# Optimization experiments

Measured on AMD Instinct MI355X. Metric: run time of the kernel, lower is better.

## Reference

```python
import jax, jax.numpy as jnp
import numpy as np

N_NODES = 100000
N_EDGES = 1600000
IN_CH, HID_CH, OUT_CH = 128, 64, 64


def setup_inputs() -> dict:
    key = jax.random.key(0)
    ks = jax.random.split(key, 6)
    x = jax.random.normal(ks[0], (N_NODES, IN_CH), dtype=jnp.float32)
    edge_index = jax.random.randint(ks[1], (2, N_EDGES), 0, N_NODES, dtype=jnp.int64)
    W1 = jax.random.normal(ks[2], (IN_CH, HID_CH), dtype=jnp.float32) / np.float32(np.sqrt(IN_CH))
    b1 = jax.random.normal(ks[3], (HID_CH,), dtype=jnp.float32) * 0.01
    W2 = jax.random.normal(ks[4], (HID_CH, OUT_CH), dtype=jnp.float32) / np.float32(np.sqrt(HID_CH))
    b2 = jax.random.normal(ks[5], (OUT_CH,), dtype=jnp.float32) * 0.01
    return {"x": x, "edge_index": edge_index, "W1": W1, "b1": b1, "W2": W2, "b2": b2}


def gcn_conv(x, W, b, src, dst, n_nodes):
    """PyG GCNConv: h = x@W; add self-loops; sym-normalized scatter-add; + bias."""
    h = x @ W  # (N, F_out)
    # degree on graph WITH self-loops (unit edge weights): deg[i] = in-degree + 1
    deg = jax.ops.segment_sum(jnp.ones((src.shape[0],), h.dtype), dst, num_segments=n_nodes) + 1.0
    dinv = jax.lax.rsqrt(deg)  # deg >= 1, no div-by-zero
    norm = dinv[src] * dinv[dst]  # (E,)
    msg = h[src] * norm[:, None]  # (E, F_out) gather + scale
    agg = jax.ops.segment_sum(msg, dst, num_segments=n_nodes)  # scatter-add
    agg = agg + h * (dinv * dinv)[:, None]  # self-loop contribution deg^-1 * h_i
    return agg + b


def reference(x, edge_index, W1, b1, W2, b2):
    src, dst = edge_index[0], edge_index[1]  # source_to_target flow
    n = x.shape[0]
    h = jax.nn.relu(gcn_conv(x, W1, b1, src, dst, n))
    out = gcn_conv(h, W2, b2, src, dst, n)
    return out
```

## Files before the change

### kernel.cpp

```cpp
#include <hip/hip_runtime.h>
#include <hip/hip_fp16.h>


#define CHUNK 2048
#define BCAP  8192
#define NB_PAD 512
#define BSHIFT 8
#define BMASK 255

typedef _Float16 f16x8 __attribute__((ext_vector_type(8)));
typedef float f32x4 __attribute__((ext_vector_type(4)));

__device__ __forceinline__ unsigned int pack2(float a, float b) {
  __half2 h = __floats2half2_rn(a, b);
  return *reinterpret_cast<unsigned int*>(&h);
}
__device__ __forceinline__ __half2 h2add(__half2 a, __half2 b) {
  return __hadd2(a, b);
}
__device__ __forceinline__ __half2 bcast_h2(unsigned int u) {
  return *reinterpret_cast<__half2*>(&u);
}

__global__ __launch_bounds__(256) void initcur_kernel(int* __restrict__ bcursor,
                                                      int nb) {
  int i = blockIdx.x * 256 + threadIdx.x;
  if (i < nb) bcursor[i] = i * BCAP;
}

__global__ __launch_bounds__(512) void chunksort_kernel(
    const int* __restrict__ src, const int* __restrict__ dst,
    int* __restrict__ bcursor, int* __restrict__ ebuck, int nE, int nb) {
  __shared__ int hist[NB_PAD];
  __shared__ int loff[NB_PAD];
  __shared__ int gbase[NB_PAD];
  __shared__ int lcur[NB_PAD];
  __shared__ int part[NB_PAD];
  __shared__ int srec[CHUNK];
  __shared__ int saddr[CHUNK];
  const int t = threadIdx.x;
  const int e0 = blockIdx.x * CHUNK;
  const int n = min(CHUNK, nE - e0);
  hist[t] = 0;
  __syncthreads();
  for (int i = t; i < n; i += 512) atomicAdd(&hist[dst[e0 + i] >> BSHIFT], 1);
  __syncthreads();
  part[t] = hist[t];
  __syncthreads();
  for (int off = 1; off < NB_PAD; off <<= 1) {
    int v = (t >= off) ? part[t - off] : 0;
    __syncthreads();
    part[t] += v;
    __syncthreads();
  }
  int excl = (t == 0) ? 0 : part[t - 1];
  loff[t] = excl;
  if (t < nb) {
    int c = hist[t];
    gbase[t] = c ? atomicAdd(&bcursor[t], c) : 0;
    lcur[t] = excl;
  }
  __syncthreads();
  for (int i = t; i < n; i += 512) {
    int d = dst[e0 + i];
    int b = d >> BSHIFT;
    int p = atomicAdd(&lcur[b], 1);
    srec[p] = src[e0 + i] | ((d & BMASK) << 17);
    saddr[p] = gbase[b] + (p - loff[b]);
  }
  __syncthreads();
  for (int i = t; i < n; i += 512) ebuck[saddr[i]] = srec[i];
}

__global__ __launch_bounds__(1024) void bscan_kernel(const int* __restrict__ bcursor,
                                                     int* __restrict__ bbase, int nb) {
  __shared__ int part[1024];
  const int t = threadIdx.x;
  int c = (t < nb) ? (bcursor[t] - t * BCAP) : 0;
  part[t] = c;
  __syncthreads();
  for (int off = 1; off < 1024; off <<= 1) {
    int v = (t >= off) ? part[t - off] : 0;
    __syncthreads();
    part[t] += v;
    __syncthreads();
  }
  if (t < nb) bbase[t] = part[t] - c;
}

__global__ __launch_bounds__(1024) void bucketsort_kernel(
    const int* __restrict__ ebuck, const int* __restrict__ bcursor,
    const int* __restrict__ bbase, int* __restrict__ esrc,
    int* __restrict__ rowptr, float* __restrict__ dinv, int N, int E, int nb) {
  __shared__ int hist[256];
  __shared__ int sc[256];
  __shared__ int rowcur[256];
  const int t = threadIdx.x;
  const int bk = blockIdx.x;
  const int base = bk * BCAP;
  const int cnt = bcursor[bk] - base;
  const int gb = bbase[bk];
  if (t < 256) hist[t] = 0;
  __syncthreads();
  for (int i = t; i < cnt; i += 1024)
    atomicAdd(&hist[(ebuck[base + i] >> 17) & BMASK], 1);
  __syncthreads();
  if (t < 256) sc[t] = hist[t];
  __syncthreads();
  for (int off = 1; off < 256; off <<= 1) {
    int v = 0;
    if (t < 256 && t >= off) v = sc[t - off];
    __syncthreads();
    if (t < 256) sc[t] += v;
    __syncthreads();
  }
  if (t < 256) {
    int excl = (t == 0) ? 0 : sc[t - 1];
    rowcur[t] = excl;
    int node = bk * 256 + t;
    if (node < N) {
      rowptr[node] = gb + excl;
      dinv[node] = rsqrtf((float)hist[t] + 1.0f);
    }
  }
  if (bk == nb - 1 && t == 0) rowptr[N] = E;
  __syncthreads();
  for (int i = t; i < cnt; i += 1024) {
    int rec = ebuck[base + i];
    int p = atomicAdd(&rowcur[(rec >> 17) & BMASK], 1);
    esrc[gb + p] = rec & 0x1FFFF;
  }
}

template <int K, bool IN_HALF>
__global__ __launch_bounds__(256) void gemm_mfma(const void* __restrict__ Xin,
                                                 const float* __restrict__ W,
                                                 const float* __restrict__ dinv,
                                                 __half* __restrict__ H, int N) {
  __shared__ __align__(16) unsigned char sA[128 * K * 2];
  __shared__ __align__(16) unsigned char sB[64 * K * 2];
  const int t = threadIdx.x;
  const int brow = blockIdx.x * 128;
  constexpr int CH = K / 8;
  for (int idx = t; idx < 128 * CH; idx += 256) {
    int r = idx / CH, c = idx - r * CH;
    int row = brow + r;
    if (row >= N) row = N - 1;
    unsigned int off = (unsigned int)((r * K + c * 8) * 2) ^ ((r & 7) << 4);
    uint4 pk;
    if constexpr (IN_HALF) {
      pk = *reinterpret_cast<const uint4*>((const __half*)Xin + (size_t)row * K + c * 8);
    } else {
      const float4* xp =
          reinterpret_cast<const float4*>((const float*)Xin + (size_t)row * K + c * 8);
      float4 f0 = xp[0], f1 = xp[1];
      pk.x = pack2(f0.x, f0.y);
      pk.y = pack2(f0.z, f0.w);
      pk.z = pack2(f1.x, f1.y);
      pk.w = pack2(f1.z, f1.w);
    }
    *reinterpret_cast<uint4*>(sA + off) = pk;
  }
  for (int idx = t; idx < K * 64; idx += 256) {
    int k = idx >> 6, n = idx & 63;
    __half h = __float2half_rn(W[idx]);
    unsigned int off = (unsigned int)((n * K + k) * 2) ^ ((n & 7) << 4);
    *reinterpret_cast<unsigned short*>(sB + off) =
        *reinterpret_cast<unsigned short*>(&h);
  }
  __syncthreads();

  const int wv = t >> 6, l = t & 63;
  const int lr = l & 15;
  const int lk = (l >> 4) * 8;
  f32x4 acc[2][4] = {};
#pragma unroll
  for (int ks = 0; ks < K / 32; ++ks) {
    f16x8 af[2], bf[4];
#pragma unroll
    for (int m = 0; m < 2; ++m) {
      int r = wv * 32 + m * 16 + lr;
      unsigned int off = (unsigned int)((r * K + ks * 32 + lk) * 2) ^ ((r & 7) << 4);
      af[m] = *reinterpret_cast<const f16x8*>(sA + off);
    }
#pragma unroll
    for (int n = 0; n < 4; ++n) {
      int cc = n * 16 + lr;
      unsigned int off = (unsigned int)((cc * K + ks * 32 + lk) * 2) ^ ((cc & 7) << 4);
      bf[n] = *reinterpret_cast<const f16x8*>(sB + off);
    }
#pragma unroll
    for (int m = 0; m < 2; ++m)
#pragma unroll
      for (int n = 0; n < 4; ++n)
        acc[m][n] = __builtin_amdgcn_mfma_f32_16x16x32_f16(af[m], bf[n], acc[m][n],
                                                           0, 0, 0);
  }
#pragma unroll
  for (int m = 0; m < 2; ++m) {
#pragma unroll
    for (int j = 0; j < 4; ++j) {
      int row = brow + wv * 32 + m * 16 + (l >> 4) * 4 + j;
      if (row < N) {
        float di = dinv[row];
#pragma unroll
        for (int n = 0; n < 4; ++n) {
          float v = acc[m][n][j] * di;
          H[(size_t)row * 64 + n * 16 + lr] = __float2half_rn(v);
        }
      }
    }
  }
}

template <bool RELU, bool OUT_HALF>
__global__ __launch_bounds__(256) void agg_kernel(const __half* __restrict__ hs,
                                                  const int* __restrict__ rowptr,
                                                  const int* __restrict__ esrc,
                                                  const float* __restrict__ dinv,
                                                  const float* __restrict__ b,
                                                  void* __restrict__ outv, int N) {
  const int wv = threadIdx.x >> 6;
  const int lane = threadIdx.x & 63;
  const int nid = lane >> 4;
  const int g = (lane >> 3) & 1;
  const int cl = lane & 7;
  const int node = blockIdx.x * 16 + wv * 4 + nid;
  const unsigned int choff = (unsigned int)cl << 4;
  const unsigned char* __restrict__ hb = (const unsigned char*)hs;
  int beg = 0, end = 0;
  if (node < N) {
    beg = rowptr[node];
    end = rowptr[node + 1];
  }
  __half2 accA[4] = {{0.f, 0.f}, {0.f, 0.f}, {0.f, 0.f}, {0.f, 0.f}};
  __half2 accB[4] = {{0.f, 0.f}, {0.f, 0.f}, {0.f, 0.f}, {0.f, 0.f}};
  int k = beg + g;
  while (k < end) {
    int s0 = esrc[min(k,     end - 1)];
    int s1 = esrc[min(k + 2, end - 1)];
    int s2 = esrc[min(k + 4, end - 1)];
    int s3 = esrc[min(k + 6, end - 1)];
    uint4 v0 = *reinterpret_cast<const uint4*>(hb + (((unsigned int)s0 << 7) + choff));
    uint4 v1 = *reinterpret_cast<const uint4*>(hb + (((unsigned int)s1 << 7) + choff));
    uint4 v2 = *reinterpret_cast<const uint4*>(hb + (((unsigned int)s2 << 7) + choff));
    uint4 v3 = *reinterpret_cast<const uint4*>(hb + (((unsigned int)s3 << 7) + choff));
    {
      accA[0] = h2add(accA[0], bcast_h2(v0.x));
      accA[1] = h2add(accA[1], bcast_h2(v0.y));
      accA[2] = h2add(accA[2], bcast_h2(v0.z));
      accA[3] = h2add(accA[3], bcast_h2(v0.w));
    }
    if (k + 2 < end) {
      accB[0] = h2add(accB[0], bcast_h2(v1.x));
      accB[1] = h2add(accB[1], bcast_h2(v1.y));
      accB[2] = h2add(accB[2], bcast_h2(v1.z));
      accB[3] = h2add(accB[3], bcast_h2(v1.w));
    }
    if (k + 4 < end) {
      accA[0] = h2add(accA[0], bcast_h2(v2.x));
      accA[1] = h2add(accA[1], bcast_h2(v2.y));
      accA[2] = h2add(accA[2], bcast_h2(v2.z));
      accA[3] = h2add(accA[3], bcast_h2(v2.w));
    }
    if (k + 6 < end) {
      accB[0] = h2add(accB[0], bcast_h2(v3.x));
      accB[1] = h2add(accB[1], bcast_h2(v3.y));
      accB[2] = h2add(accB[2], bcast_h2(v3.z));
      accB[3] = h2add(accB[3], bcast_h2(v3.w));
    }
    k += 8;
  }
#pragma unroll
  for (int r = 0; r < 4; ++r) accA[r] = h2add(accA[r], accB[r]);
#pragma unroll
  for (int r = 0; r < 4; ++r) {
    int u = __shfl_xor(*reinterpret_cast<int*>(&accA[r]), 8);
    accA[r] = h2add(accA[r], *reinterpret_cast<__half2*>(&u));
  }
  if (g == 0 && node < N) {
    uint4 sv = *reinterpret_cast<const uint4*>(hb + (((unsigned int)node << 7) + choff));
    float di = dinv[node];
    const float4* bv = reinterpret_cast<const float4*>(b);
    float4 b0 = bv[cl * 2], b1 = bv[cl * 2 + 1];
    float r[8];
#pragma unroll
    for (int q = 0; q < 4; ++q) {
      float2 av = __half22float2(accA[q]);
      float2 sf = __half22float2(bcast_h2((&sv.x)[q]));
      r[2 * q]     = (av.x + sf.x) * di;
      r[2 * q + 1] = (av.y + sf.y) * di;
    }
    r[0] += b0.x; r[1] += b0.y; r[2] += b0.z; r[3] += b0.w;
    r[4] += b1.x; r[5] += b1.y; r[6] += b1.z; r[7] += b1.w;
    if (RELU) {
#pragma unroll
      for (int q = 0; q < 8; ++q) r[q] = fmaxf(r[q], 0.f);
    }
    if constexpr (OUT_HALF) {
      uint4 pk;
      pk.x = pack2(r[0], r[1]);
      pk.y = pack2(r[2], r[3]);
      pk.z = pack2(r[4], r[5]);
      pk.w = pack2(r[6], r[7]);
      reinterpret_cast<uint4*>(outv)[(size_t)node * 8 + cl] = pk;
    } else {
      float4* ov = reinterpret_cast<float4*>(outv);
      ov[(size_t)node * 16 + cl * 2]     = make_float4(r[0], r[1], r[2], r[3]);
      ov[(size_t)node * 16 + cl * 2 + 1] = make_float4(r[4], r[5], r[6], r[7]);
    }
  }
}

extern "C" void kernel_launch(void* const* d_in, const int* in_sizes, int n_in,
                              void* d_out, int out_size, void* d_ws, size_t ws_size,
                              hipStream_t stream) {
  const float* x  = (const float*)d_in[0];
  const int*   ei = (const int*)d_in[1];
  const float* W1 = (const float*)d_in[2];
  const float* b1 = (const float*)d_in[3];
  const float* W2 = (const float*)d_in[4];
  const float* b2 = (const float*)d_in[5];
  const int N = in_sizes[0] / 128;
  const int E = in_sizes[1] / 2;
  const int* src = ei;
  const int* dst = ei + E;
  const int nb = (N + 255) >> BSHIFT;

  char* ws = (char*)d_ws;
  int*    bcursor = (int*)ws;
  int*    bbase   = (int*)(ws + (1 << 19));
  float*  dinv    = (float*)(ws + (1 << 20));
  int*    rowptr  = (int*)(ws + 3 * (1 << 19));
  int*    esrc    = (int*)(ws + (1 << 21));
  int*    ebuck   = (int*)(ws + 9 * (1 << 20));
  __half* hs      = (__half*)(ws + 22 * (1 << 20));
  __half* y1h     = (__half*)(ws + 36 * (1 << 20));
  float*  out = (float*)d_out;

  initcur_kernel<<<(nb + 255) / 256, 256, 0, stream>>>(bcursor, nb);
  chunksort_kernel<<<(E + CHUNK - 1) / CHUNK, 512, 0, stream>>>(src, dst, bcursor,
                                                                ebuck, E, nb);
  bscan_kernel<<<1, 1024, 0, stream>>>(bcursor, bbase, nb);
  bucketsort_kernel<<<nb, 1024, 0, stream>>>(ebuck, bcursor, bbase, esrc, rowptr,
                                             dinv, N, E, nb);

  const int gemmGrid = (N + 127) / 128;
  const int aggGrid = (N + 15) / 16;
  gemm_mfma<128, false><<<gemmGrid, 256, 0, stream>>>(x, W1, dinv, hs, N);
  agg_kernel<true, true><<<aggGrid, 256, 0, stream>>>(hs, rowptr, esrc, dinv, b1,
                                                      y1h, N);
  gemm_mfma<64, true><<<gemmGrid, 256, 0, stream>>>(y1h, W2, dinv, hs, N);
  agg_kernel<false, false><<<aggGrid, 256, 0, stream>>>(hs, rowptr, esrc, dinv, b2,
                                                        out, N);
}
```

Measured before the change: 144.2 us.

## Fuse layer-1 aggregation with layer-2 GEMM into one kernel

```diff
diff --git a/kernel.cpp b/kernel.cpp
--- a/kernel.cpp
+++ b/kernel.cpp
@@ -213,19 +213,29 @@
   }
 }
 
-template <bool RELU, bool OUT_HALF>
-__global__ __launch_bounds__(256) void agg_kernel(const __half* __restrict__ hs,
-                                                  const int* __restrict__ rowptr,
-                                                  const int* __restrict__ esrc,
-                                                  const float* __restrict__ dinv,
-                                                  const float* __restrict__ b,
-                                                  void* __restrict__ outv, int N) {
-  const int wv = threadIdx.x >> 6;
-  const int lane = threadIdx.x & 63;
+__global__ __launch_bounds__(256) void agg_gemm_kernel(
+    const __half* __restrict__ hs, const int* __restrict__ rowptr,
+    const int* __restrict__ esrc, const float* __restrict__ dinv,
+    const float* __restrict__ b, const float* __restrict__ W2,
+    __half* __restrict__ H2, int N) {
+  __shared__ __align__(16) unsigned char sY[16 * 64 * 2];
+  __shared__ __align__(16) unsigned char sW[64 * 64 * 2];
+  const int t = threadIdx.x;
+  for (int idx = t; idx < 64 * 64; idx += 256) {
+    int k = idx >> 6, n = idx & 63;
+    __half h = __float2half_rn(W2[idx]);
+    unsigned int off = (unsigned int)((n * 64 + k) * 2) ^ ((n & 7) << 4);
+    *reinterpret_cast<unsigned short*>(sW + off) =
+        *reinterpret_cast<unsigned short*>(&h);
+  }
+
+  const int wv = t >> 6;
+  const int lane = t & 63;
   const int nid = lane >> 4;
   const int g = (lane >> 3) & 1;
   const int cl = lane & 7;
-  const int node = blockIdx.x * 16 + wv * 4 + nid;
+  const int nodeL = wv * 4 + nid;
+  const int node = blockIdx.x * 16 + nodeL;
   const unsigned int choff = (unsigned int)cl << 4;
   const unsigned char* __restrict__ hb = (const unsigned char*)hs;
   int beg = 0, end = 0;
@@ -293,22 +303,131 @@
     }
     r[0] += b0.x; r[1] += b0.y; r[2] += b0.z; r[3] += b0.w;
     r[4] += b1.x; r[5] += b1.y; r[6] += b1.z; r[7] += b1.w;
-    if (RELU) {
-#pragma unroll
-      for (int q = 0; q < 8; ++q) r[q] = fmaxf(r[q], 0.f);
-    }
-    if constexpr (OUT_HALF) {
-      uint4 pk;
-      pk.x = pack2(r[0], r[1]);
-      pk.y = pack2(r[2], r[3]);
-      pk.z = pack2(r[4], r[5]);
-      pk.w = pack2(r[6], r[7]);
-      reinterpret_cast<uint4*>(outv)[(size_t)node * 8 + cl] = pk;
-    } else {
-      float4* ov = reinterpret_cast<float4*>(outv);
-      ov[(size_t)node * 16 + cl * 2]     = make_float4(r[0], r[1], r[2], r[3]);
-      ov[(size_t)node * 16 + cl * 2 + 1] = make_float4(r[4], r[5], r[6], r[7]);
-    }
+#pragma unroll
+    for (int q = 0; q < 8; ++q) r[q] = fmaxf(r[q], 0.f);
+    uint4 pk;
+    pk.x = pack2(r[0], r[1]);
+    pk.y = pack2(r[2], r[3]);
+    pk.z = pack2(r[4], r[5]);
+    pk.w = pack2(r[6], r[7]);
+    unsigned int off = (unsigned int)((nodeL * 64 + cl * 8) * 2) ^ ((nodeL & 7) << 4);
+    *reinterpret_cast<uint4*>(sY + off) = pk;
+  }
+  __syncthreads();
+  if (wv == 0) {
+    const int lr = lane & 15;
+    const int lk = (lane >> 4) * 8;
+    f32x4 acc[4] = {};
+#pragma unroll
+    for (int ks = 0; ks < 2; ++ks) {
+      unsigned int aoff = (unsigned int)((lr * 64 + ks * 32 + lk) * 2) ^ ((lr & 7) << 4);
+      f16x8 af = *reinterpret_cast<const f16x8*>(sY + aoff);
+#pragma unroll
+      for (int n = 0; n < 4; ++n) {
+        int cc = n * 16 + lr;
+        unsigned int boff = (unsigned int)((cc * 64 + ks * 32 + lk) * 2) ^ ((cc & 7) << 4);
+        f16x8 bf = *reinterpret_cast<const f16x8*>(sW + boff);
+        acc[n] = __builtin_amdgcn_mfma_f32_16x16x32_f16(af, bf, acc[n], 0, 0, 0);
+      }
+    }
+#pragma unroll
+    for (int j = 0; j < 4; ++j) {
+      int rowL = (lane >> 4) * 4 + j;
+      int row = blockIdx.x * 16 + rowL;
+      if (row < N) {
+        float di = dinv[row];
+#pragma unroll
+        for (int n = 0; n < 4; ++n) {
+          float v = acc[n][j] * di;
+          H2[(size_t)row * 64 + n * 16 + lr] = __float2half_rn(v);
+        }
+      }
+    }
+  }
+}
+
+__global__ __launch_bounds__(256) void agg_kernel(const __half* __restrict__ hs,
+                                                  const int* __restrict__ rowptr,
+                                                  const int* __restrict__ esrc,
+                                                  const float* __restrict__ dinv,
+                                                  const float* __restrict__ b,
+                                                  float* __restrict__ outv, int N) {
+  const int wv = threadIdx.x >> 6;
+  const int lane = threadIdx.x & 63;
+  const int nid = lane >> 4;
+  const int g = (lane >> 3) & 1;
+  const int cl = lane & 7;
+  const int node = blockIdx.x * 16 + wv * 4 + nid;
+  const unsigned int choff = (unsigned int)cl << 4;
+  const unsigned char* __restrict__ hb = (const unsigned char*)hs;
+  int beg = 0, end = 0;
+  if (node < N) {
+    beg = rowptr[node];
+    end = rowptr[node + 1];
+  }
+  __half2 accA[4] = {{0.f, 0.f}, {0.f, 0.f}, {0.f, 0.f}, {0.f, 0.f}};
+  __half2 accB[4] = {{0.f, 0.f}, {0.f, 0.f}, {0.f, 0.f}, {0.f, 0.f}};
+  int k = beg + g;
+  while (k < end) {
+    int s0 = esrc[min(k,     end - 1)];
+    int s1 = esrc[min(k + 2, end - 1)];
+    int s2 = esrc[min(k + 4, end - 1)];
+    int s3 = esrc[min(k + 6, end - 1)];
+    uint4 v0 = *reinterpret_cast<const uint4*>(hb + (((unsigned int)s0 << 7) + choff));
+    uint4 v1 = *reinterpret_cast<const uint4*>(hb + (((unsigned int)s1 << 7) + choff));
+    uint4 v2 = *reinterpret_cast<const uint4*>(hb + (((unsigned int)s2 << 7) + choff));
+    uint4 v3 = *reinterpret_cast<const uint4*>(hb + (((unsigned int)s3 << 7) + choff));
+    {
+      accA[0] = h2add(accA[0], bcast_h2(v0.x));
+      accA[1] = h2add(accA[1], bcast_h2(v0.y));
+      accA[2] = h2add(accA[2], bcast_h2(v0.z));
+      accA[3] = h2add(accA[3], bcast_h2(v0.w));
+    }
+    if (k + 2 < end) {
+      accB[0] = h2add(accB[0], bcast_h2(v1.x));
+      accB[1] = h2add(accB[1], bcast_h2(v1.y));
+      accB[2] = h2add(accB[2], bcast_h2(v1.z));
+      accB[3] = h2add(accB[3], bcast_h2(v1.w));
+    }
+    if (k + 4 < end) {
+      accA[0] = h2add(accA[0], bcast_h2(v2.x));
+      accA[1] = h2add(accA[1], bcast_h2(v2.y));
+      accA[2] = h2add(accA[2], bcast_h2(v2.z));
+      accA[3] = h2add(accA[3], bcast_h2(v2.w));
+    }
+    if (k + 6 < end) {
+      accB[0] = h2add(accB[0], bcast_h2(v3.x));
+      accB[1] = h2add(accB[1], bcast_h2(v3.y));
+      accB[2] = h2add(accB[2], bcast_h2(v3.z));
+      accB[3] = h2add(accB[3], bcast_h2(v3.w));
+    }
+    k += 8;
+  }
+#pragma unroll
+  for (int r = 0; r < 4; ++r) accA[r] = h2add(accA[r], accB[r]);
+#pragma unroll
+  for (int r = 0; r < 4; ++r) {
+    int u = __shfl_xor(*reinterpret_cast<int*>(&accA[r]), 8);
+    accA[r] = h2add(accA[r], *reinterpret_cast<__half2*>(&u));
+  }
+  if (g == 0 && node < N) {
+    uint4 sv = *reinterpret_cast<const uint4*>(hb + (((unsigned int)node << 7) + choff));
+    float di = dinv[node];
+    const float4* bv = reinterpret_cast<const float4*>(b);
+    float4 b0 = bv[cl * 2], b1 = bv[cl * 2 + 1];
+    float r[8];
+#pragma unroll
+    for (int q = 0; q < 4; ++q) {
+      float2 av = __half22float2(accA[q]);
+      float2 sf = __half22float2(bcast_h2((&sv.x)[q]));
+      r[2 * q]     = (av.x + sf.x) * di;
+      r[2 * q + 1] = (av.y + sf.y) * di;
+    }
+    r[0] += b0.x; r[1] += b0.y; r[2] += b0.z; r[3] += b0.w;
+    r[4] += b1.x; r[5] += b1.y; r[6] += b1.z; r[7] += b1.w;
+    float4* ov = reinterpret_cast<float4*>(outv);
+    ov[(size_t)node * 16 + cl * 2]     = make_float4(r[0], r[1], r[2], r[3]);
+    ov[(size_t)node * 16 + cl * 2 + 1] = make_float4(r[4], r[5], r[6], r[7]);
   }
 }
 
@@ -335,7 +454,7 @@
   int*    esrc    = (int*)(ws + (1 << 21));
   int*    ebuck   = (int*)(ws + 9 * (1 << 20));
   __half* hs      = (__half*)(ws + 22 * (1 << 20));
-  __half* y1h     = (__half*)(ws + 36 * (1 << 20));
+  __half* hs2     = (__half*)(ws + 36 * (1 << 20));
   float*  out = (float*)d_out;
 
   initcur_kernel<<<(nb + 255) / 256, 256, 0, stream>>>(bcursor, nb);
@@ -348,9 +467,7 @@
   const int gemmGrid = (N + 127) / 128;
   const int aggGrid = (N + 15) / 16;
   gemm_mfma<128, false><<<gemmGrid, 256, 0, stream>>>(x, W1, dinv, hs, N);
-  agg_kernel<true, true><<<aggGrid, 256, 0, stream>>>(hs, rowptr, esrc, dinv, b1,
-                                                      y1h, N);
-  gemm_mfma<64, true><<<gemmGrid, 256, 0, stream>>>(y1h, W2, dinv, hs, N);
-  agg_kernel<false, false><<<aggGrid, 256, 0, stream>>>(hs, rowptr, esrc, dinv, b2,
-                                                        out, N);
-}
+  agg_gemm_kernel<<<aggGrid, 256, 0, stream>>>(hs, rowptr, esrc, dinv, b1, W2,
+                                               hs2, N);
+  agg_kernel<<<aggGrid, 256, 0, stream>>>(hs2, rowptr, esrc, dinv, b2, out, N);
+}
```

Result: faster. 135.0 us (-6.4%).
